# Optimization experiments

Measured on AMD Instinct MI355X. Metric: run time of the kernel, lower is better.

Reference implementation:

```python
import jax, jax.numpy as jnp
import numpy as np

B, S, D, H = 2, 2048, 1024, 16
HD = D // H  # head dim 64
LN_EPS = 1e-12


def setup_inputs() -> dict:
    key = jax.random.key(0)
    ks = jax.random.split(key, 10)
    sc = 0.02
    return {
        "input_tensor": jax.random.normal(ks[0], (B, S, D), dtype=jnp.float32),
        "attention_mask": jnp.zeros((B, 1, 1, S), dtype=jnp.float32),
        "Wq": jax.random.normal(ks[1], (D, D), dtype=jnp.float32) * sc,
        "bq": jnp.zeros((D,), dtype=jnp.float32),
        "Wk": jax.random.normal(ks[2], (D, D), dtype=jnp.float32) * sc,
        "bk": jnp.zeros((D,), dtype=jnp.float32),
        "Wv": jax.random.normal(ks[3], (D, D), dtype=jnp.float32) * sc,
        "bv": jnp.zeros((D,), dtype=jnp.float32),
        "Wo": jax.random.normal(ks[4], (D, D), dtype=jnp.float32) * sc,
        "bo": jnp.zeros((D,), dtype=jnp.float32),
        "ln_gamma": jnp.ones((D,), dtype=jnp.float32),
        "ln_beta": jnp.zeros((D,), dtype=jnp.float32),
    }


def _split_heads(x):
    # [B,S,D] -> [B,H,S,hd]
    return x.reshape(B, S, H, HD).transpose(0, 2, 1, 3)


def reference(input_tensor, attention_mask, Wq, bq, Wk, bk, Wv, bv, Wo, bo, ln_gamma, ln_beta):
    q = _split_heads(input_tensor @ Wq + bq)
    k = _split_heads(input_tensor @ Wk + bk)
    v = _split_heads(input_tensor @ Wv + bv)
    scores = jnp.einsum("bhqd,bhkd->bhqk", q, k) / jnp.sqrt(jnp.float32(HD))
    scores = scores + attention_mask  # additive mask broadcast
    probs = jax.nn.softmax(scores, axis=-1)
    ctx = jnp.einsum("bhqk,bhkd->bhqd", probs, v)
    ctx = ctx.transpose(0, 2, 1, 3).reshape(B, S, D)
    hidden = ctx @ Wo + bo
    x = hidden + input_tensor
    mu = jnp.mean(x, axis=-1, keepdims=True)
    var = jnp.mean(jnp.square(x - mu), axis=-1, keepdims=True)
    return (x - mu) / jnp.sqrt(var + LN_EPS) * ln_gamma + ln_beta
```

## Files before the change

kernel.cpp:

```cpp
#include <hip/hip_runtime.h>
#include <stdint.h>

#define Bb 2
#define Ss 2048
#define Dd 1024
#define Hh 16
#define HD 64
#define Mtot 4096

typedef __bf16 bf16x8 __attribute__((ext_vector_type(8)));
typedef float f32x4 __attribute__((ext_vector_type(4)));
typedef float f32x16 __attribute__((ext_vector_type(16)));
typedef unsigned short ushort_t;

#if __has_builtin(__builtin_amdgcn_exp2f)
#define EXP2(x) __builtin_amdgcn_exp2f(x)
#else
#define EXP2(x) __expf((x) * 0.6931472f)
#endif

__device__ __forceinline__ float bf2f(ushort_t u) {
    union { uint32_t i; float f; } v;
    v.i = ((uint32_t)u) << 16;
    return v.f;
}

__device__ __forceinline__ ushort_t f2bf(float f) {
    union { float f; uint32_t i; } v;
    v.f = f;
    uint32_t u = v.i;
    u += 0x7FFFu + ((u >> 16) & 1u);
    return (ushort_t)(u >> 16);
}

__device__ __forceinline__ uint32_t cvtpk_bf16(float lo, float hi) {
    uint32_t r;
    asm("v_cvt_pk_bf16_f32 %0, %1, %2" : "=v"(r) : "v"(lo), "v"(hi));
    return r;
}

__device__ __forceinline__ float load_in(const void* p, size_t i, int isf32) {
    if (isf32) return ((const float*)p)[i];
    return bf2f(((const ushort_t*)p)[i]);
}

__device__ __forceinline__ void gload_lds16(const void* g, void* l) {
    __builtin_amdgcn_global_load_lds(
        (const __attribute__((address_space(1))) void*)g,
        (__attribute__((address_space(3))) void*)l, 16, 0, 0);
}

#define NVEC 525568ull
__global__ __launch_bounds__(256) void prep_k(
    const void* X, const void* mask, const void* bq, const void* bk,
    const void* bv, const void* bo, const void* g, const void* be,
    const void* Wq, const void* Wk, const void* Wv, const void* Wo,
    int* __restrict__ flag, ushort_t* __restrict__ cX,
    ushort_t* __restrict__ cMask, ushort_t* __restrict__ cB,
    ushort_t* __restrict__ wt) {
    __shared__ int sflag;
    __shared__ ushort_t tile[32][33];
    const int tid = threadIdx.x;
    {
        const int lane = tid & 63;
        if (tid < 64) {
            const ushort_t* Xu = (const ushort_t*)X;
            int local = 0;
            for (int i = lane; i < 2048; i += 64) {
                int e = (Xu[i] >> 7) & 0xFF;
                local += (e >= 0x90);
            }
            for (int off = 1; off < 64; off <<= 1) local += __shfl_xor(local, off);
            if (lane == 0) sflag = (local >= 4) ? 1 : 0;
        }
    }
    __syncthreads();
    const int f = sflag;
    if (blockIdx.x == 0 && tid == 0) *flag = f;

    if (blockIdx.x < 1024) {
        const size_t stride = 1024ull * 256ull;
        for (size_t t = (size_t)blockIdx.x * 256 + tid; t < NVEC; t += stride) {
            const void* src;
            ushort_t* dst;
            size_t v;
            if (t < 524288ull) {
                src = X; dst = cX; v = t;
            } else if (t < 524800ull) {
                src = mask; dst = cMask; v = t - 524288ull;
            } else {
                size_t j = t - 524800ull;
                int w = (int)(j >> 7);
                src = (w == 0) ? bq : (w == 1) ? bk : (w == 2) ? bv
                    : (w == 3) ? bo : (w == 4) ? g : be;
                dst = cB + w * 1024;
                v = j & 127;
            }
            if (f) {
                const float4* s4 = (const float4*)src;
                float4 a = s4[v * 2], b = s4[v * 2 + 1];
                union { ushort_t u[8]; uint4 q; } pk;
                pk.u[0] = f2bf(a.x); pk.u[1] = f2bf(a.y);
                pk.u[2] = f2bf(a.z); pk.u[3] = f2bf(a.w);
                pk.u[4] = f2bf(b.x); pk.u[5] = f2bf(b.y);
                pk.u[6] = f2bf(b.z); pk.u[7] = f2bf(b.w);
                ((uint4*)dst)[v] = pk.q;
            } else {
                ((uint4*)dst)[v] = ((const uint4*)src)[v];
            }
        }
    } else {
        int id2 = blockIdx.x - 1024;
        int z = id2 >> 10;
        int rem = id2 & 1023;
        int bx = rem & 31, by = rem >> 5;
        const void* W = (z == 0) ? Wq : (z == 1) ? Wk : (z == 2) ? Wv : Wo;
        ushort_t* T = wt + (size_t)z * Dd * Dd;
        int tx = tid & 31, ty = tid >> 5;
        int x = bx * 32 + tx;
        int y0 = by * 32;
        for (int i = 0; i < 4; i++) {
            int y = y0 + ty + i * 8;
            tile[ty + i * 8][tx] = f2bf(load_in(W, (size_t)y * Dd + x, f));
        }
        __syncthreads();
        int x2 = by * 32 + tx;
        int y20 = bx * 32;
        for (int i = 0; i < 4; i++) {
            int y = y20 + ty + i * 8;
            T[(size_t)y * Dd + x2] = tile[tx][ty + i * 8];
        }
    }
}

__global__ __launch_bounds__(256) void gemm_qkv(
    const ushort_t* __restrict__ X, const ushort_t* __restrict__ wt,
    const ushort_t* __restrict__ cB,
    ushort_t* __restrict__ Qb, ushort_t* __restrict__ Kb, ushort_t* __restrict__ Vtb) {
    const int z = blockIdx.z;
    const ushort_t* Wt = wt + (size_t)z * Dd * Dd;
    const ushort_t* bias = cB + z * 1024;

    __shared__ __align__(16) ushort_t smem[2][2][128 * 32];

    const int tid = threadIdx.x;
    const int lane = tid & 63, wv = tid >> 6;
    const int quad = lane >> 4, l15 = lane & 15;
    const int wrow = (wv >> 1) * 64, wcol = (wv & 1) * 64;
    const int row0 = blockIdx.y * 128, col0 = blockIdx.x * 128;
    const int lrow = lane >> 2, lcol = (lane & 3) * 8;

    const f32x4 fzero = {0.f, 0.f, 0.f, 0.f};
    f32x4 acc[4][4];
    for (int mt = 0; mt < 4; mt++)
        for (int nt = 0; nt < 4; nt++) acc[mt][nt] = fzero;

    for (int j = 0; j < 2; j++) {
        int ch = wv * 2 + j;
        gload_lds16(&X[(size_t)(row0 + ch * 16 + lrow) * Dd + lcol],
                    &smem[0][0][ch * 512]);
        gload_lds16(&Wt[(size_t)(col0 + ch * 16 + lrow) * Dd + lcol],
                    &smem[0][1][ch * 512]);
    }

    for (int k0 = 0; k0 < Dd; k0 += 32) {
        const int buf = (k0 >> 5) & 1;
        __syncthreads();
        if (k0 + 32 < Dd) {
            for (int j = 0; j < 2; j++) {
                int ch = wv * 2 + j;
                gload_lds16(&X[(size_t)(row0 + ch * 16 + lrow) * Dd + k0 + 32 + lcol],
                            &smem[buf ^ 1][0][ch * 512]);
                gload_lds16(&Wt[(size_t)(col0 + ch * 16 + lrow) * Dd + k0 + 32 + lcol],
                            &smem[buf ^ 1][1][ch * 512]);
            }
        }
        const ushort_t* As = &smem[buf][0][0];
        const ushort_t* Bs = &smem[buf][1][0];
        bf16x8 af[4], bfr[4];
        for (int mt = 0; mt < 4; mt++)
            af[mt] = *(const bf16x8*)(&As[(wrow + mt * 16 + l15) * 32 + quad * 8]);
        for (int nt = 0; nt < 4; nt++)
            bfr[nt] = *(const bf16x8*)(&Bs[(wcol + nt * 16 + l15) * 32 + quad * 8]);
        for (int mt = 0; mt < 4; mt++)
            for (int nt = 0; nt < 4; nt++)
                acc[mt][nt] = __builtin_amdgcn_mfma_f32_16x16x32_bf16(
                    af[mt], bfr[nt], acc[mt][nt], 0, 0, 0);
    }

    const float qscale = 0.18033688f;
    ushort_t* Cs = &smem[0][0][0];
    for (int mt = 0; mt < 4; mt++) {
        __syncthreads();
        for (int nt = 0; nt < 4; nt++) {
            int gn = col0 + wcol + nt * 16 + l15;
            float bv_ = bf2f(bias[gn]);
            for (int r = 0; r < 4; r++) {
                float v = acc[mt][nt][r] + bv_;
                if (z == 0) v *= qscale;
                int ric = (wv >> 1) * 16 + quad * 4 + r;
                Cs[ric * 136 + wcol + nt * 16 + l15] = f2bf(v);
            }
        }
        __syncthreads();
        if (z == 2) {
            int c = tid >> 1, r0 = (tid & 1) * 16;
            int gn = col0 + c, h = gn >> 6, d = gn & 63;
            int gmbase = row0 + (r0 >> 4) * 64 + mt * 16;
            int b = gmbase >> 11, s0 = gmbase & 2047;
            union { ushort_t u[16]; uint4 q[2]; } pk;
            for (int i = 0; i < 16; i++) pk.u[i] = Cs[(r0 + i) * 136 + c];
            uint4* dst = (uint4*)&Vtb[((size_t)((b * Hh + h) * HD + d)) * Ss + s0];
            dst[0] = pk.q[0];
            dst[1] = pk.q[1];
        } else {
            int ric = tid >> 3, c0 = (tid & 7) * 16;
            int gm = row0 + (ric >> 4) * 64 + mt * 16 + (ric & 15);
            int gn = col0 + c0, h = gn >> 6, d0 = gn & 63;
            int b = gm >> 11, s = gm & 2047;
            const uint4* src = (const uint4*)&Cs[ric * 136 + c0];
            ushort_t* Ob = (z == 0) ? Qb : Kb;
            uint4* dst = (uint4*)&Ob[((size_t)((b * Hh + h) * Ss + s)) * HD + d0];
            dst[0] = src[0];
            dst[1] = src[1];
        }
    }
}

__global__ __launch_bounds__(256, 2) void attn(
    const ushort_t* __restrict__ Q, const ushort_t* __restrict__ K,
    const ushort_t* __restrict__ Vt, const ushort_t* __restrict__ mask,
    ushort_t* __restrict__ ctx) {
    const int tid = threadIdx.x;
    const int lane = tid & 63, wv = tid >> 6;
    const int n = lane & 31, hi = lane >> 5;
    const int bh = blockIdx.x;
    const int b = bh >> 4, h = bh & 15;
    const int q0 = blockIdx.y * 128 + wv * 32;

    const ushort_t* Qh = Q + (size_t)bh * Ss * HD;
    const ushort_t* Kh = K + (size_t)bh * Ss * HD;
    const ushort_t* Vh = Vt + (size_t)bh * HD * Ss;

    __shared__ __align__(16) ushort_t Ks[2][64 * 64];
    __shared__ __align__(16) ushort_t Vs[2][64 * 64];
    __shared__ __align__(16) float maskF[Ss];

    for (int i = tid; i < Ss; i += 256)
        maskF[i] = (bf2f(mask[b * Ss + i]) - 4.0f) * 1.4426950f;

    const int r8 = lane >> 3, c8 = lane & 7, gc = c8 ^ r8;
    const int sw = n & 7;

    for (int j = 0; j < 2; j++) {
        int row = wv * 16 + j * 8;
        gload_lds16(&Kh[(size_t)(row + r8) * HD + gc * 8], &Ks[0][row * 64]);
        gload_lds16(&Vh[(size_t)(row + r8) * Ss + gc * 8], &Vs[0][row * 64]);
    }

    bf16x8 qf[4];
#pragma unroll
    for (int ks = 0; ks < 4; ks++)
        qf[ks] = *(const bf16x8*)(&Qh[(size_t)(q0 + n) * HD + ks * 16 + hi * 8]);

    bf16x8 onesf;
    {
        union { ushort_t u[8]; bf16x8 v; } ou;
        for (int i = 0; i < 8; i++) ou.u[i] = 0x3F80;
        onesf = ou.v;
    }

    f32x16 o[2], o_l;
#pragma unroll
    for (int r = 0; r < 16; r++) { o[0][r] = 0.f; o[1][r] = 0.f; o_l[r] = 0.f; }

    for (int kb = 0; kb < Ss; kb += 64) {
        const int buf = (kb >> 6) & 1;
        __syncthreads();

        if (kb + 64 < Ss) {
            for (int j = 0; j < 2; j++) {
                int row = wv * 16 + j * 8;
                gload_lds16(&Kh[(size_t)(kb + 64 + row + r8) * HD + gc * 8],
                            &Ks[buf ^ 1][row * 64]);
                gload_lds16(&Vh[(size_t)(row + r8) * Ss + kb + 64 + gc * 8],
                            &Vs[buf ^ 1][row * 64]);
            }
        }

        const ushort_t* ks_ = &Ks[buf][0];
        const ushort_t* vs_ = &Vs[buf][0];

        f32x16 st[2];
#pragma unroll
        for (int mt = 0; mt < 2; mt++) {
#pragma unroll
            for (int r4 = 0; r4 < 4; r4++) {
                f32x4 mk = *(const f32x4*)(&maskF[kb + mt * 32 + r4 * 8 + hi * 4]);
                st[mt][r4 * 4 + 0] = mk[0];
                st[mt][r4 * 4 + 1] = mk[1];
                st[mt][r4 * 4 + 2] = mk[2];
                st[mt][r4 * 4 + 3] = mk[3];
            }
        }
        __builtin_amdgcn_s_setprio(1);
#pragma unroll
        for (int mt = 0; mt < 2; mt++) {
#pragma unroll
            for (int ksp = 0; ksp < 4; ksp++) {
                bf16x8 kf = *(const bf16x8*)(
                    &ks_[(mt * 32 + n) * 64 + ((ksp * 2 + hi) ^ sw) * 8]);
                st[mt] = __builtin_amdgcn_mfma_f32_32x32x16_bf16(
                    kf, qf[ksp], st[mt], 0, 0, 0);
            }
        }
        __builtin_amdgcn_s_setprio(0);

#pragma unroll
        for (int mt = 0; mt < 2; mt++)
#pragma unroll
            for (int r = 0; r < 16; r++) st[mt][r] = EXP2(st[mt][r]);

#pragma unroll
        for (int c = 0; c < 4; c++) {
            const int mt = c >> 1, cc = (c & 1) * 8;
            uint32_t a0 = cvtpk_bf16(st[mt][cc + 0], st[mt][cc + 1]);
            uint32_t a1 = cvtpk_bf16(st[mt][cc + 2], st[mt][cc + 3]);
            uint32_t b0 = cvtpk_bf16(st[mt][cc + 4], st[mt][cc + 5]);
            uint32_t b1 = cvtpk_bf16(st[mt][cc + 6], st[mt][cc + 7]);
            asm("v_permlane32_swap_b32 %0, %1" : "+v"(a0), "+v"(b0));
            asm("v_permlane32_swap_b32 %0, %1" : "+v"(a1), "+v"(b1));
            union { uint32_t w[4]; bf16x8 v; } pa;
            pa.w[0] = a0; pa.w[1] = a1; pa.w[2] = b0; pa.w[3] = b1;
            __builtin_amdgcn_s_setprio(1);
#pragma unroll
            for (int dt = 0; dt < 2; dt++) {
                bf16x8 vf = *(const bf16x8*)(
                    &vs_[(dt * 32 + n) * 64 + ((c * 2 + hi) ^ sw) * 8]);
                o[dt] = __builtin_amdgcn_mfma_f32_32x32x16_bf16(
                    pa.v, vf, o[dt], 0, 0, 0);
            }
            o_l = __builtin_amdgcn_mfma_f32_32x32x16_bf16(
                pa.v, onesf, o_l, 0, 0, 0);
            __builtin_amdgcn_s_setprio(0);
        }
    }

#pragma unroll
    for (int r = 0; r < 16; r++) {
        int q = q0 + (r & 3) + 8 * (r >> 2) + 4 * hi;
        float linv = 1.f / o_l[r];
#pragma unroll
        for (int dt = 0; dt < 2; dt++) {
            ctx[((size_t)(b * Ss + q)) * Dd + h * HD + dt * 32 + n] =
                f2bf(o[dt][r] * linv);
        }
    }
}

__global__ __launch_bounds__(256) void gemm_out(
    const ushort_t* __restrict__ A, const ushort_t* __restrict__ Wt,
    const ushort_t* __restrict__ bo, const ushort_t* __restrict__ X,
    ushort_t* __restrict__ xout) {
    __shared__ __align__(16) ushort_t smem[2][6144];

    const int tid = threadIdx.x;
    const int lane = tid & 63, wv = tid >> 6;
    const int quad = lane >> 4, l15 = lane & 15;
    const int wrow = (wv >> 1) * 32, wcol = (wv & 1) * 64;
    const int row0 = blockIdx.y * 64, col0 = blockIdx.x * 128;
    const int lrow = lane >> 2, lcol = (lane & 3) * 8;

    const f32x4 fzero = {0.f, 0.f, 0.f, 0.f};
    f32x4 acc[2][4];
    for (int mt = 0; mt < 2; mt++)
        for (int nt = 0; nt < 4; nt++) acc[mt][nt] = fzero;

    gload_lds16(&A[(size_t)(row0 + wv * 16 + lrow) * Dd + lcol], &smem[0][wv * 512]);
    for (int j = 0; j < 2; j++) {
        int ch = wv * 2 + j;
        gload_lds16(&Wt[(size_t)(col0 + ch * 16 + lrow) * Dd + lcol],
                    &smem[0][2048 + ch * 512]);
    }

    for (int k0 = 0; k0 < Dd; k0 += 32) {
        const int buf = (k0 >> 5) & 1;
        __syncthreads();
        if (k0 + 32 < Dd) {
            gload_lds16(&A[(size_t)(row0 + wv * 16 + lrow) * Dd + k0 + 32 + lcol],
                        &smem[buf ^ 1][wv * 512]);
            for (int j = 0; j < 2; j++) {
                int ch = wv * 2 + j;
                gload_lds16(&Wt[(size_t)(col0 + ch * 16 + lrow) * Dd + k0 + 32 + lcol],
                            &smem[buf ^ 1][2048 + ch * 512]);
            }
        }
        const ushort_t* As = &smem[buf][0];
        const ushort_t* Bs = &smem[buf][2048];
        bf16x8 af[2], bfr[4];
        for (int mt = 0; mt < 2; mt++)
            af[mt] = *(const bf16x8*)(&As[(wrow + mt * 16 + l15) * 32 + quad * 8]);
        for (int nt = 0; nt < 4; nt++)
            bfr[nt] = *(const bf16x8*)(&Bs[(wcol + nt * 16 + l15) * 32 + quad * 8]);
        for (int mt = 0; mt < 2; mt++)
            for (int nt = 0; nt < 4; nt++)
                acc[mt][nt] = __builtin_amdgcn_mfma_f32_16x16x32_bf16(
                    af[mt], bfr[nt], acc[mt][nt], 0, 0, 0);
    }

    for (int mt = 0; mt < 2; mt++)
        for (int nt = 0; nt < 4; nt++)
            for (int r = 0; r < 4; r++) {
                int gm = row0 + wrow + mt * 16 + quad * 4 + r;
                int gn = col0 + wcol + nt * 16 + l15;
                float v = acc[mt][nt][r] + bf2f(bo[gn]) + bf2f(X[(size_t)gm * Dd + gn]);
                xout[(size_t)gm * Dd + gn] = f2bf(v);
            }
}

__global__ __launch_bounds__(256) void ln_k(
    const ushort_t* __restrict__ x, const ushort_t* __restrict__ gamma,
    const ushort_t* __restrict__ beta, const int* __restrict__ flag,
    void* __restrict__ out) {
    const int row = blockIdx.x;
    const int tid = threadIdx.x;
    const int f = *flag;

    union { uint2 q; ushort_t u[4]; } xv;
    xv.q = ((const uint2*)(x + (size_t)row * Dd))[tid];
    float xi[4];
    for (int i = 0; i < 4; i++) xi[i] = bf2f(xv.u[i]);
    float s = (xi[0] + xi[1]) + (xi[2] + xi[3]);
    float ss = (xi[0] * xi[0] + xi[1] * xi[1]) + (xi[2] * xi[2] + xi[3] * xi[3]);
    for (int off = 1; off < 64; off <<= 1) {
        s += __shfl_xor(s, off);
        ss += __shfl_xor(ss, off);
    }
    __shared__ float ps[4], pss[4];
    int wv = tid >> 6;
    if ((tid & 63) == 0) { ps[wv] = s; pss[wv] = ss; }
    __syncthreads();
    s = ps[0] + ps[1] + ps[2] + ps[3];
    ss = pss[0] + pss[1] + pss[2] + pss[3];
    float mu = s * (1.f / Dd);
    float var = ss * (1.f / Dd) - mu * mu;
    float rstd = rsqrtf(fmaxf(var, 0.f) + 1e-12f);

    const int c0 = tid * 4;
    float r[4];
    for (int i = 0; i < 4; i++) {
        float g = bf2f(gamma[c0 + i]);
        float bb = bf2f(beta[c0 + i]);
        r[i] = (xi[i] - mu) * rstd * g + bb;
    }
    if (f) {
        float4 o4 = {r[0], r[1], r[2], r[3]};
        ((float4*)out)[(size_t)row * 256 + tid] = o4;
    } else {
        union { ushort_t u[4]; uint2 q; } pk;
        for (int i = 0; i < 4; i++) pk.u[i] = f2bf(r[i]);
        *(uint2*)((ushort_t*)out + (size_t)row * Dd + c0) = pk.q;
    }
}

extern "C" void kernel_launch(void* const* d_in, const int* in_sizes, int n_in,
                              void* d_out, int out_size, void* d_ws, size_t ws_size,
                              hipStream_t stream) {
    char* ws = (char*)d_ws;
    int* flag       = (int*)ws;
    ushort_t* cMask = (ushort_t*)(ws + (64ull << 10));
    ushort_t* cB    = (ushort_t*)(ws + (96ull << 10));
    ushort_t* cX    = (ushort_t*)(ws + (1ull << 20));
    ushort_t* wt    = (ushort_t*)(ws + (17ull << 20));
    ushort_t* Qb    = (ushort_t*)(ws + (25ull << 20));
    ushort_t* Kb    = (ushort_t*)(ws + (33ull << 20));
    ushort_t* Vtb   = (ushort_t*)(ws + (41ull << 20));
    ushort_t* ctx   = (ushort_t*)(ws + (49ull << 20));
    ushort_t* xbuf  = (ushort_t*)(ws + (25ull << 20));

    hipLaunchKernelGGL(prep_k, dim3(5120), dim3(256), 0, stream,
                       d_in[0], d_in[1], d_in[3], d_in[5], d_in[7], d_in[9],
                       d_in[10], d_in[11], d_in[2], d_in[4], d_in[6], d_in[8],
                       flag, cX, cMask, cB, wt);
    hipLaunchKernelGGL(gemm_qkv, dim3(8, 32, 3), dim3(256), 0, stream,
                       cX, wt, cB, Qb, Kb, Vtb);
    hipLaunchKernelGGL(attn, dim3(32, 16), dim3(256), 0, stream,
                       Qb, Kb, Vtb, cMask, ctx);
    hipLaunchKernelGGL(gemm_out, dim3(8, 64), dim3(256), 0, stream,
                       ctx, wt + 3ull * Dd * Dd, cB + 3 * 1024, cX, xbuf);
    hipLaunchKernelGGL(ln_k, dim3(Mtot), dim3(256), 0, stream,
                       xbuf, cB + 4 * 1024, cB + 5 * 1024, flag, d_out);
}
```

Measured before the change: 205.0 us.

## Process two query tiles per wave in attention to reuse K/V fragments

Each attention wave now handles two 32-row query tiles (offset by 128) instead of one, so every K and V fragment read from LDS feeds two MFMAs and the K/V tile loads are amortized over twice as many queries. The grid's query dimension is halved to 256 blocks and launch bounds drop to one block per SIMD to allow the doubled accumulator register footprint. This trades occupancy and grid parallelism (256 blocks on a many-CU device) for higher arithmetic intensity per LDS load.

```diff
diff --git a/kernel.cpp b/kernel.cpp
--- a/kernel.cpp
+++ b/kernel.cpp
@@ -227,7 +227,7 @@
     }
 }
 
-__global__ __launch_bounds__(256, 2) void attn(
+__global__ __launch_bounds__(256, 1) void attn(
     const ushort_t* __restrict__ Q, const ushort_t* __restrict__ K,
     const ushort_t* __restrict__ Vt, const ushort_t* __restrict__ mask,
     ushort_t* __restrict__ ctx) {
@@ -236,7 +236,8 @@
     const int n = lane & 31, hi = lane >> 5;
     const int bh = blockIdx.x;
     const int b = bh >> 4, h = bh & 15;
-    const int q0 = blockIdx.y * 128 + wv * 32;
+    const int q0 = blockIdx.y * 256 + wv * 32;
+    const int q1 = q0 + 128;
 
     const ushort_t* Qh = Q + (size_t)bh * Ss * HD;
     const ushort_t* Kh = K + (size_t)bh * Ss * HD;
@@ -258,10 +259,12 @@
         gload_lds16(&Vh[(size_t)(row + r8) * Ss + gc * 8], &Vs[0][row * 64]);
     }
 
-    bf16x8 qf[4];
-#pragma unroll
-    for (int ks = 0; ks < 4; ks++)
-        qf[ks] = *(const bf16x8*)(&Qh[(size_t)(q0 + n) * HD + ks * 16 + hi * 8]);
+    bf16x8 qfA[4], qfB[4];
+#pragma unroll
+    for (int ks = 0; ks < 4; ks++) {
+        qfA[ks] = *(const bf16x8*)(&Qh[(size_t)(q0 + n) * HD + ks * 16 + hi * 8]);
+        qfB[ks] = *(const bf16x8*)(&Qh[(size_t)(q1 + n) * HD + ks * 16 + hi * 8]);
+    }
 
     bf16x8 onesf;
     {
@@ -270,9 +273,12 @@
         onesf = ou.v;
     }
 
-    f32x16 o[2], o_l;
-#pragma unroll
-    for (int r = 0; r < 16; r++) { o[0][r] = 0.f; o[1][r] = 0.f; o_l[r] = 0.f; }
+    f32x16 oA[2], oB[2], olA, olB;
+#pragma unroll
+    for (int r = 0; r < 16; r++) {
+        oA[0][r] = 0.f; oA[1][r] = 0.f; oB[0][r] = 0.f; oB[1][r] = 0.f;
+        olA[r] = 0.f; olB[r] = 0.f;
+    }
 
     for (int kb = 0; kb < Ss; kb += 64) {
         const int buf = (kb >> 6) & 1;
@@ -291,16 +297,17 @@
         const ushort_t* ks_ = &Ks[buf][0];
         const ushort_t* vs_ = &Vs[buf][0];
 
-        f32x16 st[2];
+        f32x16 stA[2], stB[2];
 #pragma unroll
         for (int mt = 0; mt < 2; mt++) {
 #pragma unroll
             for (int r4 = 0; r4 < 4; r4++) {
                 f32x4 mk = *(const f32x4*)(&maskF[kb + mt * 32 + r4 * 8 + hi * 4]);
-                st[mt][r4 * 4 + 0] = mk[0];
-                st[mt][r4 * 4 + 1] = mk[1];
-                st[mt][r4 * 4 + 2] = mk[2];
-                st[mt][r4 * 4 + 3] = mk[3];
+#pragma unroll
+                for (int j = 0; j < 4; j++) {
+                    stA[mt][r4 * 4 + j] = mk[j];
+                    stB[mt][r4 * 4 + j] = mk[j];
+                }
             }
         }
         __builtin_amdgcn_s_setprio(1);
@@ -310,8 +317,10 @@
             for (int ksp = 0; ksp < 4; ksp++) {
                 bf16x8 kf = *(const bf16x8*)(
                     &ks_[(mt * 32 + n) * 64 + ((ksp * 2 + hi) ^ sw) * 8]);
-                st[mt] = __builtin_amdgcn_mfma_f32_32x32x16_bf16(
-                    kf, qf[ksp], st[mt], 0, 0, 0);
+                stA[mt] = __builtin_amdgcn_mfma_f32_32x32x16_bf16(
+                    kf, qfA[ksp], stA[mt], 0, 0, 0);
+                stB[mt] = __builtin_amdgcn_mfma_f32_32x32x16_bf16(
+                    kf, qfB[ksp], stB[mt], 0, 0, 0);
             }
         }
         __builtin_amdgcn_s_setprio(0);
@@ -319,41 +328,61 @@
 #pragma unroll
         for (int mt = 0; mt < 2; mt++)
 #pragma unroll
-            for (int r = 0; r < 16; r++) st[mt][r] = EXP2(st[mt][r]);
+            for (int r = 0; r < 16; r++) {
+                stA[mt][r] = EXP2(stA[mt][r]);
+                stB[mt][r] = EXP2(stB[mt][r]);
+            }
 
 #pragma unroll
         for (int c = 0; c < 4; c++) {
             const int mt = c >> 1, cc = (c & 1) * 8;
-            uint32_t a0 = cvtpk_bf16(st[mt][cc + 0], st[mt][cc + 1]);
-            uint32_t a1 = cvtpk_bf16(st[mt][cc + 2], st[mt][cc + 3]);
-            uint32_t b0 = cvtpk_bf16(st[mt][cc + 4], st[mt][cc + 5]);
-            uint32_t b1 = cvtpk_bf16(st[mt][cc + 6], st[mt][cc + 7]);
-            asm("v_permlane32_swap_b32 %0, %1" : "+v"(a0), "+v"(b0));
-            asm("v_permlane32_swap_b32 %0, %1" : "+v"(a1), "+v"(b1));
-            union { uint32_t w[4]; bf16x8 v; } pa;
-            pa.w[0] = a0; pa.w[1] = a1; pa.w[2] = b0; pa.w[3] = b1;
+            uint32_t a0A = cvtpk_bf16(stA[mt][cc + 0], stA[mt][cc + 1]);
+            uint32_t a1A = cvtpk_bf16(stA[mt][cc + 2], stA[mt][cc + 3]);
+            uint32_t b0A = cvtpk_bf16(stA[mt][cc + 4], stA[mt][cc + 5]);
+            uint32_t b1A = cvtpk_bf16(stA[mt][cc + 6], stA[mt][cc + 7]);
+            asm("v_permlane32_swap_b32 %0, %1" : "+v"(a0A), "+v"(b0A));
+            asm("v_permlane32_swap_b32 %0, %1" : "+v"(a1A), "+v"(b1A));
+            union { uint32_t w[4]; bf16x8 v; } paA;
+            paA.w[0] = a0A; paA.w[1] = a1A; paA.w[2] = b0A; paA.w[3] = b1A;
+
+            uint32_t a0B = cvtpk_bf16(stB[mt][cc + 0], stB[mt][cc + 1]);
+            uint32_t a1B = cvtpk_bf16(stB[mt][cc + 2], stB[mt][cc + 3]);
+            uint32_t b0B = cvtpk_bf16(stB[mt][cc + 4], stB[mt][cc + 5]);
+            uint32_t b1B = cvtpk_bf16(stB[mt][cc + 6], stB[mt][cc + 7]);
+            asm("v_permlane32_swap_b32 %0, %1" : "+v"(a0B), "+v"(b0B));
+            asm("v_permlane32_swap_b32 %0, %1" : "+v"(a1B), "+v"(b1B));
+            union { uint32_t w[4]; bf16x8 v; } paB;
+            paB.w[0] = a0B; paB.w[1] = a1B; paB.w[2] = b0B; paB.w[3] = b1B;
+
             __builtin_amdgcn_s_setprio(1);
 #pragma unroll
             for (int dt = 0; dt < 2; dt++) {
                 bf16x8 vf = *(const bf16x8*)(
                     &vs_[(dt * 32 + n) * 64 + ((c * 2 + hi) ^ sw) * 8]);
-                o[dt] = __builtin_amdgcn_mfma_f32_32x32x16_bf16(
-                    pa.v, vf, o[dt], 0, 0, 0);
-            }
-            o_l = __builtin_amdgcn_mfma_f32_32x32x16_bf16(
-                pa.v, onesf, o_l, 0, 0, 0);
+                oA[dt] = __builtin_amdgcn_mfma_f32_32x32x16_bf16(
+                    paA.v, vf, oA[dt], 0, 0, 0);
+                oB[dt] = __builtin_amdgcn_mfma_f32_32x32x16_bf16(
+                    paB.v, vf, oB[dt], 0, 0, 0);
+            }
+            olA = __builtin_amdgcn_mfma_f32_32x32x16_bf16(
+                paA.v, onesf, olA, 0, 0, 0);
+            olB = __builtin_amdgcn_mfma_f32_32x32x16_bf16(
+                paB.v, onesf, olB, 0, 0, 0);
             __builtin_amdgcn_s_setprio(0);
         }
     }
 
 #pragma unroll
     for (int r = 0; r < 16; r++) {
-        int q = q0 + (r & 3) + 8 * (r >> 2) + 4 * hi;
-        float linv = 1.f / o_l[r];
+        int qa = q0 + (r & 3) + 8 * (r >> 2) + 4 * hi;
+        float linvA = 1.f / olA[r];
+        float linvB = 1.f / olB[r];
 #pragma unroll
         for (int dt = 0; dt < 2; dt++) {
-            ctx[((size_t)(b * Ss + q)) * Dd + h * HD + dt * 32 + n] =
-                f2bf(o[dt][r] * linv);
+            ctx[((size_t)(b * Ss + qa)) * Dd + h * HD + dt * 32 + n] =
+                f2bf(oA[dt][r] * linvA);
+            ctx[((size_t)(b * Ss + qa + 128)) * Dd + h * HD + dt * 32 + n] =
+                f2bf(oB[dt][r] * linvB);
         }
     }
 }
@@ -484,7 +513,7 @@
                        flag, cX, cMask, cB, wt);
     hipLaunchKernelGGL(gemm_qkv, dim3(8, 32, 3), dim3(256), 0, stream,
                        cX, wt, cB, Qb, Kb, Vtb);
-    hipLaunchKernelGGL(attn, dim3(32, 16), dim3(256), 0, stream,
+    hipLaunchKernelGGL(attn, dim3(32, 8), dim3(256), 0, stream,
                        Qb, Kb, Vtb, cMask, ctx);
     hipLaunchKernelGGL(gemm_out, dim3(8, 64), dim3(256), 0, stream,
                        ctx, wt + 3ull * Dd * Dd, cB + 3 * 1024, cX, xbuf);
```

New measurement: 226.2 us. 10.3% more time.

## Software-pipeline attention loop: overlap exp of previous tile with QK MFMAs

Applied to the files above, without the earlier changes.

Restructures the attention inner loop into a two-stage software pipeline. The QK^T MFMAs for tile t are interleaved with the exp2 of tile t-1's scores, and then the PV MFMAs for tile t-1 run. V fragments for each tile are loaded into registers before the next barrier so the double-buffered LDS can be reused. The aim is to hide transcendental VALU latency behind matrix-core work, at the cost of more live registers (two score sets plus eight V fragments), which could cause spills at 2 waves per SIMD.

```diff
diff --git a/kernel.cpp b/kernel.cpp
--- a/kernel.cpp
+++ b/kernel.cpp
@@ -227,6 +227,82 @@
     }
 }
 
+#define ATTN_ITER(T, PREV, CUR, DOPV, DOSTAGE)                                \
+  {                                                                           \
+    const int t_ = (T);                                                       \
+    const int kb_ = t_ * 64;                                                  \
+    const int bufc_ = t_ & 1;                                                 \
+    __syncthreads();                                                          \
+    if (DOSTAGE) {                                                            \
+      _Pragma("unroll")                                                       \
+      for (int j = 0; j < 2; j++) {                                           \
+        int row = wv * 16 + j * 8;                                            \
+        gload_lds16(&Kh[(size_t)(kb_ + 64 + row + r8) * HD + gc * 8],         \
+                    &Ks[bufc_ ^ 1][row * 64]);                                \
+        gload_lds16(&Vh[(size_t)(row + r8) * Ss + kb_ + 64 + gc * 8],         \
+                    &Vs[bufc_ ^ 1][row * 64]);                                \
+      }                                                                       \
+    }                                                                         \
+    const ushort_t* ks_ = &Ks[bufc_][0];                                      \
+    const ushort_t* vs_ = &Vs[bufc_][0];                                      \
+    _Pragma("unroll")                                                         \
+    for (int mt = 0; mt < 2; mt++) {                                          \
+      _Pragma("unroll")                                                       \
+      for (int r4 = 0; r4 < 4; r4++) {                                        \
+        f32x4 mk = *(const f32x4*)(&maskF[kb_ + mt * 32 + r4 * 8 + hi * 4]);  \
+        CUR[mt][r4 * 4 + 0] = mk[0];                                          \
+        CUR[mt][r4 * 4 + 1] = mk[1];                                          \
+        CUR[mt][r4 * 4 + 2] = mk[2];                                          \
+        CUR[mt][r4 * 4 + 3] = mk[3];                                          \
+      }                                                                       \
+    }                                                                         \
+    __builtin_amdgcn_s_setprio(1);                                            \
+    _Pragma("unroll")                                                         \
+    for (int u = 0; u < 8; u++) {                                             \
+      const int ksp_ = u >> 1, mt_ = u & 1;                                   \
+      bf16x8 kf = *(const bf16x8*)(                                           \
+          &ks_[(mt_ * 32 + n) * 64 + ((ksp_ * 2 + hi) ^ sw) * 8]);            \
+      CUR[mt_] = __builtin_amdgcn_mfma_f32_32x32x16_bf16(                     \
+          kf, qf[ksp_], CUR[mt_], 0, 0, 0);                                   \
+      if (DOPV) {                                                             \
+        PREV[0][u * 2 + 0] = EXP2(PREV[0][u * 2 + 0]);                        \
+        PREV[0][u * 2 + 1] = EXP2(PREV[0][u * 2 + 1]);                        \
+        PREV[1][u * 2 + 0] = EXP2(PREV[1][u * 2 + 0]);                        \
+        PREV[1][u * 2 + 1] = EXP2(PREV[1][u * 2 + 1]);                        \
+      }                                                                       \
+    }                                                                         \
+    __builtin_amdgcn_s_setprio(0);                                            \
+    if (DOPV) {                                                               \
+      _Pragma("unroll")                                                       \
+      for (int c = 0; c < 4; c++) {                                           \
+        const int mt_ = c >> 1, cc_ = (c & 1) * 8;                            \
+        uint32_t a0 = cvtpk_bf16(PREV[mt_][cc_ + 0], PREV[mt_][cc_ + 1]);     \
+        uint32_t a1 = cvtpk_bf16(PREV[mt_][cc_ + 2], PREV[mt_][cc_ + 3]);     \
+        uint32_t b0 = cvtpk_bf16(PREV[mt_][cc_ + 4], PREV[mt_][cc_ + 5]);     \
+        uint32_t b1 = cvtpk_bf16(PREV[mt_][cc_ + 6], PREV[mt_][cc_ + 7]);     \
+        asm("v_permlane32_swap_b32 %0, %1" : "+v"(a0), "+v"(b0));             \
+        asm("v_permlane32_swap_b32 %0, %1" : "+v"(a1), "+v"(b1));             \
+        union { uint32_t w[4]; bf16x8 v; } pa;                                \
+        pa.w[0] = a0; pa.w[1] = a1; pa.w[2] = b0; pa.w[3] = b1;               \
+        __builtin_amdgcn_s_setprio(1);                                        \
+        _Pragma("unroll")                                                     \
+        for (int dt = 0; dt < 2; dt++)                                        \
+          o[dt] = __builtin_amdgcn_mfma_f32_32x32x16_bf16(                    \
+              pa.v, vfr[c * 2 + dt], o[dt], 0, 0, 0);                         \
+        o_l = __builtin_amdgcn_mfma_f32_32x32x16_bf16(                        \
+            pa.v, onesf, o_l, 0, 0, 0);                                       \
+        __builtin_amdgcn_s_setprio(0);                                        \
+      }                                                                       \
+    }                                                                         \
+    _Pragma("unroll")                                                         \
+    for (int c = 0; c < 4; c++) {                                             \
+      _Pragma("unroll")                                                       \
+      for (int dt = 0; dt < 2; dt++)                                          \
+        vfr[c * 2 + dt] = *(const bf16x8*)(                                   \
+            &vs_[(dt * 32 + n) * 64 + ((c * 2 + hi) ^ sw) * 8]);              \
+    }                                                                         \
+  }
+
 __global__ __launch_bounds__(256, 2) void attn(
     const ushort_t* __restrict__ Q, const ushort_t* __restrict__ K,
     const ushort_t* __restrict__ Vt, const ushort_t* __restrict__ mask,
@@ -274,76 +350,36 @@
 #pragma unroll
     for (int r = 0; r < 16; r++) { o[0][r] = 0.f; o[1][r] = 0.f; o_l[r] = 0.f; }
 
-    for (int kb = 0; kb < Ss; kb += 64) {
-        const int buf = (kb >> 6) & 1;
-        __syncthreads();
-
-        if (kb + 64 < Ss) {
-            for (int j = 0; j < 2; j++) {
-                int row = wv * 16 + j * 8;
-                gload_lds16(&Kh[(size_t)(kb + 64 + row + r8) * HD + gc * 8],
-                            &Ks[buf ^ 1][row * 64]);
-                gload_lds16(&Vh[(size_t)(row + r8) * Ss + kb + 64 + gc * 8],
-                            &Vs[buf ^ 1][row * 64]);
-            }
-        }
-
-        const ushort_t* ks_ = &Ks[buf][0];
-        const ushort_t* vs_ = &Vs[buf][0];
-
-        f32x16 st[2];
-#pragma unroll
-        for (int mt = 0; mt < 2; mt++) {
-#pragma unroll
-            for (int r4 = 0; r4 < 4; r4++) {
-                f32x4 mk = *(const f32x4*)(&maskF[kb + mt * 32 + r4 * 8 + hi * 4]);
-                st[mt][r4 * 4 + 0] = mk[0];
-                st[mt][r4 * 4 + 1] = mk[1];
-                st[mt][r4 * 4 + 2] = mk[2];
-                st[mt][r4 * 4 + 3] = mk[3];
-            }
-        }
-        __builtin_amdgcn_s_setprio(1);
-#pragma unroll
-        for (int mt = 0; mt < 2; mt++) {
-#pragma unroll
-            for (int ksp = 0; ksp < 4; ksp++) {
-                bf16x8 kf = *(const bf16x8*)(
-                    &ks_[(mt * 32 + n) * 64 + ((ksp * 2 + hi) ^ sw) * 8]);
-                st[mt] = __builtin_amdgcn_mfma_f32_32x32x16_bf16(
-                    kf, qf[ksp], st[mt], 0, 0, 0);
-            }
-        }
-        __builtin_amdgcn_s_setprio(0);
-
-#pragma unroll
-        for (int mt = 0; mt < 2; mt++)
-#pragma unroll
-            for (int r = 0; r < 16; r++) st[mt][r] = EXP2(st[mt][r]);
-
-#pragma unroll
-        for (int c = 0; c < 4; c++) {
-            const int mt = c >> 1, cc = (c & 1) * 8;
-            uint32_t a0 = cvtpk_bf16(st[mt][cc + 0], st[mt][cc + 1]);
-            uint32_t a1 = cvtpk_bf16(st[mt][cc + 2], st[mt][cc + 3]);
-            uint32_t b0 = cvtpk_bf16(st[mt][cc + 4], st[mt][cc + 5]);
-            uint32_t b1 = cvtpk_bf16(st[mt][cc + 6], st[mt][cc + 7]);
-            asm("v_permlane32_swap_b32 %0, %1" : "+v"(a0), "+v"(b0));
-            asm("v_permlane32_swap_b32 %0, %1" : "+v"(a1), "+v"(b1));
-            union { uint32_t w[4]; bf16x8 v; } pa;
-            pa.w[0] = a0; pa.w[1] = a1; pa.w[2] = b0; pa.w[3] = b1;
-            __builtin_amdgcn_s_setprio(1);
-#pragma unroll
-            for (int dt = 0; dt < 2; dt++) {
-                bf16x8 vf = *(const bf16x8*)(
-                    &vs_[(dt * 32 + n) * 64 + ((c * 2 + hi) ^ sw) * 8]);
-                o[dt] = __builtin_amdgcn_mfma_f32_32x32x16_bf16(
-                    pa.v, vf, o[dt], 0, 0, 0);
-            }
-            o_l = __builtin_amdgcn_mfma_f32_32x32x16_bf16(
-                pa.v, onesf, o_l, 0, 0, 0);
-            __builtin_amdgcn_s_setprio(0);
-        }
+    f32x16 stA[2], stB[2];
+    bf16x8 vfr[8];
+
+    ATTN_ITER(0, stB, stA, 0, 1)
+    for (int it2 = 0; it2 < 15; it2++) {
+        ATTN_ITER(2 * it2 + 1, stA, stB, 1, 1)
+        ATTN_ITER(2 * it2 + 2, stB, stA, 1, 1)
+    }
+    ATTN_ITER(31, stA, stB, 1, 0)
+
+#pragma unroll
+    for (int mt = 0; mt < 2; mt++)
+#pragma unroll
+        for (int r = 0; r < 16; r++) stB[mt][r] = EXP2(stB[mt][r]);
+#pragma unroll
+    for (int c = 0; c < 4; c++) {
+        const int mt = c >> 1, cc = (c & 1) * 8;
+        uint32_t a0 = cvtpk_bf16(stB[mt][cc + 0], stB[mt][cc + 1]);
+        uint32_t a1 = cvtpk_bf16(stB[mt][cc + 2], stB[mt][cc + 3]);
+        uint32_t b0 = cvtpk_bf16(stB[mt][cc + 4], stB[mt][cc + 5]);
+        uint32_t b1 = cvtpk_bf16(stB[mt][cc + 6], stB[mt][cc + 7]);
+        asm("v_permlane32_swap_b32 %0, %1" : "+v"(a0), "+v"(b0));
+        asm("v_permlane32_swap_b32 %0, %1" : "+v"(a1), "+v"(b1));
+        union { uint32_t w[4]; bf16x8 v; } pa;
+        pa.w[0] = a0; pa.w[1] = a1; pa.w[2] = b0; pa.w[3] = b1;
+#pragma unroll
+        for (int dt = 0; dt < 2; dt++)
+            o[dt] = __builtin_amdgcn_mfma_f32_32x32x16_bf16(
+                pa.v, vfr[c * 2 + dt], o[dt], 0, 0, 0);
+        o_l = __builtin_amdgcn_mfma_f32_32x32x16_bf16(pa.v, onesf, o_l, 0, 0, 0);
     }
 
 #pragma unroll
```

Measured after the change: 204.4 us. No clear change (-0.3%).
